# Performance work log

Hardware: AMD Instinct MI355X
Metric: run time of the kernel (lower is better)

The kernel has to match this reference:

```python
import jax, jax.numpy as jnp
import numpy as np

B, FEAT, H, W = 16, 64, 32, 32


def setup_inputs() -> dict:
    key = jax.random.key(0)
    ks = jax.random.split(key, 8)
    s = 0.05
    return {
        "x": jax.random.normal(ks[0], (B, 2 * FEAT, H, W), jnp.float32),
        # i2s_conv: MaskConv(2F -> 4F, 1x1, maskB with group=1 == all-ones), bias=False
        "w_i2s": jax.random.normal(ks[1], (4 * FEAT, 2 * FEAT), jnp.float32) * s,
        # left/right state-to-state Conv2d(F -> 4F, kernel (2,1)), with bias
        "w_left": jax.random.normal(ks[2], (4 * FEAT, FEAT, 2), jnp.float32) * s,
        "b_left": jax.random.normal(ks[3], (4 * FEAT,), jnp.float32) * s,
        "w_right": jax.random.normal(ks[4], (4 * FEAT, FEAT, 2), jnp.float32) * s,
        "b_right": jax.random.normal(ks[5], (4 * FEAT,), jnp.float32) * s,
        # skip_conv: MaskConv(F -> 2F, 1x1, maskB group=1 == plain conv), bias=True
        "w_skip": jax.random.normal(ks[6], (2 * FEAT, FEAT), jnp.float32) * s,
        "b_skip": jax.random.normal(ks[7], (2 * FEAT,), jnp.float32) * s,
    }


def _shift_right_w(a):  # F.pad(a,(1,0,...))[..., :-1]
    return jnp.pad(a, ((0, 0), (0, 0), (0, 0), (1, 0)))[:, :, :, :-1]


def _shift_left_w(a):  # F.pad(a,(0,1,...))[..., 1:]
    return jnp.pad(a, ((0, 0), (0, 0), (0, 0), (0, 1)))[:, :, :, 1:]


def _shift_down_h(a):  # pad one row on top, drop last row
    return jnp.pad(a, ((0, 0), (0, 0), (1, 0), (0, 0)))[:, :, :-1, :]


def _s2s(hprev, w, b, wshift):
    # pad(top=1, side=1) + Conv2d kernel (2,1) + crop one column, expressed as
    # two 1x1 contractions on width-shifted / (width+height)-shifted maps.
    hw = wshift(hprev)            # [B,F,H,W] shifted one column
    hd = _shift_down_h(hw)        # additionally shifted one row down
    return (jnp.einsum('bchw,oc->bohw', hd, w[:, :, 0])
            + jnp.einsum('bchw,oc->bohw', hw, w[:, :, 1])
            + b[None, :, None, None])


def _forward(x, w_i2s, w_left, b_left, w_right, b_right, w_skip, b_skip):
    b_, c2, h_, w_ = x.shape
    f = c2 // 2
    hmap = jnp.einsum('bchw,oc->bohw', x, w_i2s)  # [B,4F,H,W]
    left_h = hmap   # stew: input-to-state shared between directions
    right_h = hmap
    zeros = jnp.zeros((b_, f, h_, w_), x.dtype)

    def step(carry, _):
        lc, lh, rc, rh = carry
        pre = jax.nn.sigmoid(_s2s(lh, w_left, b_left, _shift_right_w) + left_h)
        o, fg, ig, g = jnp.split(pre, 4, axis=1)
        lc = fg * lc + ig * g
        lh = o * jnp.tanh(lc)
        pre = jax.nn.sigmoid(_s2s(rh, w_right, b_right, _shift_left_w) + right_h)
        o, fg, ig, g = jnp.split(pre, 4, axis=1)
        rc = fg * rc + ig * g
        rh = o * jnp.tanh(rc)
        return (lc, lh, rc, rh), None

    (lc, lh, rc, rh), _ = jax.lax.scan(step, (zeros, zeros, zeros, zeros), None, length=h_)
    rh = _shift_down_h(rh)  # unstew + shift right stream down one row
    out_h = lh + rh         # [B,F,H,W]
    skip = jnp.einsum('bchw,oc->bohw', out_h, w_skip) + b_skip[None, :, None, None]
    return x + skip


def reference(x, w_i2s, w_left, b_left, w_right, b_right, w_skip, b_skip):
    return _forward(x, w_i2s, w_left, b_left, w_right, b_right, w_skip, b_skip)
```

## Files before the change

kernel.cpp:

```cpp
#include <hip/hip_runtime.h>


using bf16   = __bf16;
using bf16x8 = __attribute__((ext_vector_type(8))) __bf16;
using f32x4  = __attribute__((ext_vector_type(4))) float;

#define SCOPE_AGENT __HIP_MEMORY_SCOPE_AGENT
#define LOG2E 1.4426950408889634f
#define K2E   2.8853900817779268f

__device__ __forceinline__ bf16x8 bzero8() {
  bf16x8 v;
#pragma unroll
  for (int e = 0; e < 8; ++e) v[e] = (bf16)0.0f;
  return v;
}
__device__ __forceinline__ unsigned short f2bu(float f) {
  bf16 b = (bf16)f;
  return __builtin_bit_cast(unsigned short, b);
}
__device__ __forceinline__ float bu2f(unsigned short u) {
  return __uint_as_float(((unsigned)u) << 16);
}

__global__ void prep_kernel(const float* __restrict__ w_i2s,
                            const float* __restrict__ w_left,
                            const float* __restrict__ w_right,
                            const float* __restrict__ w_skip,
                            bf16* __restrict__ WnI, bf16* __restrict__ WnL,
                            bf16* __restrict__ WnR, bf16* __restrict__ WnS) {
  int t = blockIdx.x * 256 + threadIdx.x;
  if (t < 32768) {
    WnI[t] = (bf16)w_i2s[t];
    int o = t >> 7, k = t & 127;
    int src = (k < 64) ? (o * 128 + k * 2) : (o * 128 + (k - 64) * 2 + 1);
    WnL[t] = (bf16)(w_left[src] * LOG2E);
    WnR[t] = (bf16)(w_right[src] * LOG2E);
    if (t < 8192) WnS[t] = (bf16)w_skip[t];
  }
}

__global__ __launch_bounds__(256, 2)
void hmap_kernel(const float* __restrict__ x, const bf16* __restrict__ Wn,
                 const float* __restrict__ bL, const float* __restrict__ bR,
                 ushort4* __restrict__ hmapL, ushort4* __restrict__ hmapR) {
  __shared__ __align__(16) bf16 At[64 * 128];
  const int tile = blockIdx.x;
  const int b = tile >> 4, h0 = (tile & 15) << 1;
  const int t = threadIdx.x;
  const float* xb = x + (size_t)(b * 128) * 1024 + h0 * 32;
#pragma unroll
  for (int i = 0; i < 8; ++i) {
    int idx = t + 256 * i;
    int cc = idx >> 4, m4 = idx & 15;
    f32x4 v = *(const f32x4*)(xb + (size_t)cc * 1024 + m4 * 4);
#pragma unroll
    for (int e = 0; e < 4; ++e) {
      int m = m4 * 4 + e;
      int kb = (cc * 2) ^ ((m & 7) << 4);
      *(bf16*)((char*)At + m * 256 + kb) = (bf16)v[e];
    }
  }
  __syncthreads();
  const int wv = t >> 6, l = t & 63;
  const int l15 = l & 15, lq = l >> 4;
  const int c = wv * 16 + l15;
  bf16x8 bfrag[4][4];
#pragma unroll
  for (int g = 0; g < 4; ++g)
#pragma unroll
    for (int kk = 0; kk < 4; ++kk)
      bfrag[g][kk] = *(const bf16x8*)(Wn + (g * 64 + c) * 128 + kk * 32 + lq * 8);
  float blq[4], brq[4];
#pragma unroll
  for (int g = 0; g < 4; ++g) {
    blq[g] = bL[g * 64 + c] * LOG2E;
    brq[g] = bR[g * 64 + c] * LOG2E;
  }
  f32x4 acc[4][4];
  const f32x4 fz = {0.f, 0.f, 0.f, 0.f};
#pragma unroll
  for (int ms = 0; ms < 4; ++ms)
#pragma unroll
    for (int g = 0; g < 4; ++g) acc[ms][g] = fz;
#pragma unroll
  for (int kk = 0; kk < 4; ++kk) {
#pragma unroll
    for (int ms = 0; ms < 4; ++ms) {
      int m = ms * 16 + l15;
      int kb = ((kk * 32 + lq * 8) * 2) ^ ((m & 7) << 4);
      bf16x8 a = *(const bf16x8*)((const char*)At + m * 256 + kb);
#pragma unroll
      for (int g = 0; g < 4; ++g)
        acc[ms][g] =
            __builtin_amdgcn_mfma_f32_16x16x32_bf16(a, bfrag[g][kk], acc[ms][g], 0, 0, 0);
    }
  }
  const int pix0 = tile * 64;
#pragma unroll
  for (int ms = 0; ms < 4; ++ms)
#pragma unroll
    for (int j = 0; j < 4; ++j) {
      int p = pix0 + ms * 16 + lq * 4 + j;
      ushort4 hl, hr;
      float a0 = acc[ms][0][j] * LOG2E, a1 = acc[ms][1][j] * LOG2E;
      float a2 = acc[ms][2][j] * LOG2E, a3 = acc[ms][3][j] * LOG2E;
      hl.x = f2bu(a0 + blq[0]); hl.y = f2bu(a1 + blq[1]);
      hl.z = f2bu(a2 + blq[2]); hl.w = f2bu(a3 + blq[3]);
      hr.x = f2bu(a0 + brq[0]); hr.y = f2bu(a1 + brq[1]);
      hr.z = f2bu(a2 + brq[2]); hr.w = f2bu(a3 + brq[3]);
      hmapL[(size_t)p * 64 + c] = hl;
      hmapR[(size_t)p * 64 + c] = hr;
    }
}

__global__ __launch_bounds__(512, 4)
void scan_kernel(bf16* __restrict__ lhLout, bf16* __restrict__ lhRout,
                 const ushort4* __restrict__ hmapL,
                 const ushort4* __restrict__ hmapR,
                 const bf16* __restrict__ WnL, const bf16* __restrict__ WnR,
                 bf16* __restrict__ ring, unsigned* __restrict__ prodFlag,
                 unsigned* __restrict__ consFlag) {
  __shared__ __align__(16) bf16 buf[2][3 * 32 * 64];
  __shared__ __align__(16) ushort4 hlds[64 * 64];
  const int blk = blockIdx.x;
  const int q = blk & 31, tl = blk >> 5;
  const bool right = (q & 1) != 0;
  const int b = q >> 1;
  const int r0 = tl * 2;
  const int t = threadIdx.x;
  const int dw = right ? 1 : -1;
  bf16* __restrict__ lout = right ? lhRout : lhLout;
  const bf16* __restrict__ Wn = right ? WnR : WnL;
  const ushort4* __restrict__ hsrc =
      (right ? hmapR : hmapL) + (size_t)(b * 1024 + r0 * 32) * 64;
  const int w8 = t >> 6, l = t & 63, l15 = l & 15, lq = l >> 4;
  const int wv = w8 & 3, mhalf = w8 >> 2;
  const int c = wv * 16 + l15;
  const int wb_ = mhalf * 16;

#pragma unroll
  for (int i = 0; i < 8; ++i) hlds[t + 512 * i] = hsrc[t + 512 * i];

#pragma unroll
  for (int i = 0; i < 2; ++i) {
    int idx = t + 512 * i;
    if (idx < 768) ((bf16x8*)buf[0])[idx] = bzero8();
  }
  if (t < 256) ((bf16x8*)buf[1])[t] = bzero8();

  bf16x8 bfrag[4][4];
#pragma unroll
  for (int g = 0; g < 4; ++g)
#pragma unroll
    for (int kk = 0; kk < 4; ++kk)
      bfrag[g][kk] = *(const bf16x8*)(Wn + (g * 64 + c) * 128 + kk * 32 + lq * 8);
  float lcA[4], lcB[4];
#pragma unroll
  for (int j = 0; j < 4; ++j) {
    lcA[j] = 0.0f;
    lcB[j] = 0.0f;
  }

  const unsigned* pBelow = prodFlag + (size_t)(blk - 32) * 32;
  const unsigned* cAbove = consFlag + (size_t)(blk + 32) * 32;
  unsigned* myProd = prodFlag + (size_t)blk * 32;
  unsigned* myCons = consFlag + (size_t)blk * 32;

  const int wsrc = wb_ + l15 + dw;
  const bool oob = (unsigned)wsrc >= 32u;
  const int wc = wsrc & 31;
  const int swz = (wc & 7) << 4;

  __syncthreads();

#pragma unroll 1
  for (int s = 0; s < 32; ++s) {
    bf16* curb = buf[s & 1];
    bf16* nxtb = buf[(s + 1) & 1];
    const bool consume = (tl > 0) && (s > 0);
    const bool publish = (tl < 15) && (s < 31);
    bf16* slotOut = ring + (size_t)(((s & 3) * 512) + blk) * 2048;

    if (publish && s >= 4) {
      const unsigned tgt = (unsigned)(s - 3);
      while (__hip_atomic_load(cAbove, __ATOMIC_RELAXED, SCOPE_AGENT) < tgt)
        __builtin_amdgcn_s_sleep(1);
    }

    {
      f32x4 acc[4];
      const f32x4 fz = {0.f, 0.f, 0.f, 0.f};
#pragma unroll
      for (int g = 0; g < 4; ++g) acc[g] = fz;
#pragma unroll
      for (int kk = 0; kk < 4; ++kk) {
        const int srcr = 1 + (kk >> 1);
        const int c0 = (kk & 1) * 32 + lq * 8;
        int aoff = ((srcr * 32 + wc) * 128 + c0 * 2) ^ swz;
        bf16x8 a = *(const bf16x8*)((const char*)curb + aoff);
        if (oob) a = bzero8();
#pragma unroll
        for (int g = 0; g < 4; ++g)
          acc[g] = __builtin_amdgcn_mfma_f32_16x16x32_bf16(a, bfrag[g][kk], acc[g], 0, 0, 0);
      }
#pragma unroll
      for (int j = 0; j < 4; ++j) {
        const int w = wb_ + lq * 4 + j;
        ushort4 hm = hlds[(32 + w) * 64 + c];
        float e0 = __builtin_amdgcn_exp2f(-(acc[0][j] + bu2f(hm.x)));
        float e1 = __builtin_amdgcn_exp2f(-(acc[1][j] + bu2f(hm.y)));
        float e2 = __builtin_amdgcn_exp2f(-(acc[2][j] + bu2f(hm.z)));
        float e3 = __builtin_amdgcn_exp2f(-(acc[3][j] + bu2f(hm.w)));
        float fg = __builtin_amdgcn_rcpf(1.0f + e1);
        float igg = __builtin_amdgcn_rcpf((1.0f + e2) * (1.0f + e3));
        float lcv = fg * lcA[j] + K2E * igg;
        lcA[j] = lcv;
        float ey = __builtin_amdgcn_exp2f(-lcv);
        float lh = (1.0f - ey) * __builtin_amdgcn_rcpf((1.0f + e0) * (1.0f + ey));
        bf16 vb = (bf16)lh;
        int woff = ((2 * 32 + w) * 128 + c * 2) ^ ((w & 7) << 4);
        *(bf16*)((char*)nxtb + woff) = vb;
        if (publish) {
          unsigned u = (unsigned)__builtin_bit_cast(unsigned short, vb);
          unsigned pv = (unsigned)__shfl_xor((int)u, 1);
          if ((l & 1) == 0) {
            unsigned dword = u | (pv << 16);
            __hip_atomic_store((unsigned*)(slotOut + w * 64 + (c & ~1)), dword,
                               __ATOMIC_RELAXED, SCOPE_AGENT);
          }
        }
      }
    }
    __syncthreads();
    if (publish && t == 0)
      __hip_atomic_store(myProd, (unsigned)(s + 1), __ATOMIC_RELAXED, SCOPE_AGENT);

    if (consume) {
      const unsigned tgt = (unsigned)s;
      while (__hip_atomic_load(pBelow, __ATOMIC_RELAXED, SCOPE_AGENT) < tgt)
        __builtin_amdgcn_s_sleep(1);
      if (t < 256) {
        const bf16* slotIn =
            ring + (size_t)((((s - 1) & 3) * 512) + (blk - 32)) * 2048;
        int w = t >> 3, c8 = t & 7;
        const unsigned long long* src =
            (const unsigned long long*)(slotIn + w * 64 + c8 * 8);
        unsigned long long d0 = __hip_atomic_load(src, __ATOMIC_RELAXED, SCOPE_AGENT);
        unsigned long long d1 = __hip_atomic_load(src + 1, __ATOMIC_RELAXED, SCOPE_AGENT);
        int off = (w * 128 + c8 * 16) ^ ((w & 7) << 4);
        *(unsigned long long*)((char*)curb + off) = d0;
        *(unsigned long long*)((char*)curb + off + 8) = d1;
      }
    }
    __syncthreads();
    if (consume && t == 0)
      __hip_atomic_store(myCons, (unsigned)s, __ATOMIC_RELAXED, SCOPE_AGENT);

    {
      f32x4 acc[4];
      const f32x4 fz = {0.f, 0.f, 0.f, 0.f};
#pragma unroll
      for (int g = 0; g < 4; ++g) acc[g] = fz;
#pragma unroll
      for (int kk = 0; kk < 4; ++kk) {
        const int srcr = kk >> 1;
        const int c0 = (kk & 1) * 32 + lq * 8;
        int aoff = ((srcr * 32 + wc) * 128 + c0 * 2) ^ swz;
        bf16x8 a = *(const bf16x8*)((const char*)curb + aoff);
        if (oob) a = bzero8();
#pragma unroll
        for (int g = 0; g < 4; ++g)
          acc[g] = __builtin_amdgcn_mfma_f32_16x16x32_bf16(a, bfrag[g][kk], acc[g], 0, 0, 0);
      }
#pragma unroll
      for (int j = 0; j < 4; ++j) {
        const int w = wb_ + lq * 4 + j;
        ushort4 hm = hlds[w * 64 + c];
        float e0 = __builtin_amdgcn_exp2f(-(acc[0][j] + bu2f(hm.x)));
        float e1 = __builtin_amdgcn_exp2f(-(acc[1][j] + bu2f(hm.y)));
        float e2 = __builtin_amdgcn_exp2f(-(acc[2][j] + bu2f(hm.z)));
        float e3 = __builtin_amdgcn_exp2f(-(acc[3][j] + bu2f(hm.w)));
        float fg = __builtin_amdgcn_rcpf(1.0f + e1);
        float igg = __builtin_amdgcn_rcpf((1.0f + e2) * (1.0f + e3));
        float lcv = fg * lcB[j] + K2E * igg;
        lcB[j] = lcv;
        float ey = __builtin_amdgcn_exp2f(-lcv);
        float lh = (1.0f - ey) * __builtin_amdgcn_rcpf((1.0f + e0) * (1.0f + ey));
        int woff = ((1 * 32 + w) * 128 + c * 2) ^ ((w & 7) << 4);
        *(bf16*)((char*)nxtb + woff) = (bf16)lh;
      }
    }
    __syncthreads();
  }

  {
    int R = 1 + (t >> 8), rem = t & 255;
    int w = rem >> 3, c8 = rem & 7;
    int off = ((R * 32 + w) * 128 + c8 * 16) ^ ((w & 7) << 4);
    bf16x8 v = *(const bf16x8*)((const char*)buf[0] + off);
    *(bf16x8*)(lout + (size_t)((b * 32 + r0 + R - 1) * 32 + w) * 64 + c8 * 8) = v;
  }
}

__global__ __launch_bounds__(256, 2)
void final_kernel(const float* __restrict__ x, const bf16* __restrict__ lhL,
                  const bf16* __restrict__ lhR, const bf16* __restrict__ Wn,
                  const float* __restrict__ b_skip, float* __restrict__ out) {
  __shared__ __align__(16) bf16 At[64 * 64];
  __shared__ __align__(16) float smemT[128 * 72];
  const int tile = blockIdx.x;
  const int b = tile >> 4, h0 = (tile & 15) << 1;
  const int t = threadIdx.x;
#pragma unroll
  for (int i = 0; i < 2; ++i) {
    int idx = t + 256 * i;
    int m = idx >> 3, c8 = idx & 7;
    int h = h0 + (m >> 5), w = m & 31;
    size_t p = (size_t)(b * 32 + h) * 32 + w;
    bf16x8 vL = *(const bf16x8*)(lhL + p * 64 + c8 * 8);
    bf16x8 v;
    if (h > 0) {
      bf16x8 vR = *(const bf16x8*)(lhR + (p - 32) * 64 + c8 * 8);
#pragma unroll
      for (int e = 0; e < 8; ++e) v[e] = (bf16)((float)vL[e] + (float)vR[e]);
    } else {
      v = vL;
    }
    int kb = (c8 * 16) ^ ((m & 7) << 4);
    *(bf16x8*)((char*)At + m * 128 + kb) = v;
  }
  __syncthreads();
  const int wv = t >> 6, l = t & 63;
  const int l15 = l & 15, lq = l >> 4;
  const int c = wv * 16 + l15;
  bf16x8 bfrag[2][2];
#pragma unroll
  for (int g = 0; g < 2; ++g)
#pragma unroll
    for (int kk = 0; kk < 2; ++kk)
      bfrag[g][kk] = *(const bf16x8*)(Wn + (g * 64 + c) * 64 + kk * 32 + lq * 8);
  f32x4 acc[4][2];
  const f32x4 fz = {0.f, 0.f, 0.f, 0.f};
#pragma unroll
  for (int ms = 0; ms < 4; ++ms)
#pragma unroll
    for (int g = 0; g < 2; ++g) acc[ms][g] = fz;
#pragma unroll
  for (int kk = 0; kk < 2; ++kk) {
#pragma unroll
    for (int ms = 0; ms < 4; ++ms) {
      int m = ms * 16 + l15;
      int kb = ((kk * 32 + lq * 8) * 2) ^ ((m & 7) << 4);
      bf16x8 a = *(const bf16x8*)((const char*)At + m * 128 + kb);
#pragma unroll
      for (int g = 0; g < 2; ++g)
        acc[ms][g] =
            __builtin_amdgcn_mfma_f32_16x16x32_bf16(a, bfrag[g][kk], acc[ms][g], 0, 0, 0);
    }
  }
  float bsk[2];
#pragma unroll
  for (int g = 0; g < 2; ++g) bsk[g] = b_skip[g * 64 + c];
#pragma unroll
  for (int ms = 0; ms < 4; ++ms)
#pragma unroll
    for (int g = 0; g < 2; ++g)
#pragma unroll
      for (int j = 0; j < 4; ++j) {
        int m = ms * 16 + lq * 4 + j;
        int n = g * 64 + c;
        smemT[n * 72 + m] = acc[ms][g][j] + bsk[g];
      }
  __syncthreads();
  const float* xb = x + (size_t)(b * 128) * 1024 + h0 * 32;
  float* ob = out + (size_t)(b * 128) * 1024 + h0 * 32;
#pragma unroll
  for (int i = 0; i < 8; ++i) {
    int idx = t + 256 * i;
    int o2 = idx >> 4, m4 = idx & 15;
    f32x4 s = *(const f32x4*)(&smemT[o2 * 72 + m4 * 4]);
    f32x4 xv = *(const f32x4*)(xb + (size_t)o2 * 1024 + m4 * 4);
#pragma unroll
    for (int e = 0; e < 4; ++e) s[e] += xv[e];
    *(f32x4*)(ob + (size_t)o2 * 1024 + m4 * 4) = s;
  }
}

extern "C" void kernel_launch(void* const* d_in, const int* in_sizes, int n_in,
                              void* d_out, int out_size, void* d_ws, size_t ws_size,
                              hipStream_t stream) {
  const float* x       = (const float*)d_in[0];
  const float* w_i2s   = (const float*)d_in[1];
  const float* w_left  = (const float*)d_in[2];
  const float* b_left  = (const float*)d_in[3];
  const float* w_right = (const float*)d_in[4];
  const float* b_right = (const float*)d_in[5];
  const float* w_skip  = (const float*)d_in[6];
  const float* b_skip  = (const float*)d_in[7];
  float* out = (float*)d_out;
  char* ws = (char*)d_ws;

  bf16*     lhL   = (bf16*)(ws + 0x0000000);
  bf16*     lhR   = (bf16*)(ws + 0x0200000);
  ushort4*  hmapL = (ushort4*)(ws + 0x0400000);
  ushort4*  hmapR = (ushort4*)(ws + 0x0C00000);
  bf16*     ring  = (bf16*)(ws + 0x1400000);
  unsigned* prodF = (unsigned*)(ws + 0x1C00000);
  unsigned* consF = (unsigned*)(ws + 0x1C10000);
  bf16*     WnI   = (bf16*)(ws + 0x1C20000);
  bf16*     WnL   = (bf16*)(ws + 0x1C30000);
  bf16*     WnR   = (bf16*)(ws + 0x1C40000);
  bf16*     WnS   = (bf16*)(ws + 0x1C50000);

  hipMemsetAsync(ws + 0x1C00000, 0, 0x20000, stream);
  prep_kernel<<<128, 256, 0, stream>>>(w_i2s, w_left, w_right, w_skip, WnI, WnL, WnR, WnS);
  hmap_kernel<<<256, 256, 0, stream>>>(x, WnI, b_left, b_right, hmapL, hmapR);
  scan_kernel<<<512, 512, 0, stream>>>(lhL, lhR, hmapL, hmapR, WnL, WnR,
                                       ring, prodF, consF);
  final_kernel<<<256, 256, 0, stream>>>(x, lhL, lhR, WnS, b_skip, out);
}
```

Measured before the change: 173.9 us.

## Hoist ring consume before first half-step, seed MFMA accumulators with hmap, pad LDS

The cross-block ring read for the row below now happens at the start of each step, spread over all 512 threads. This removes one __syncthreads per step and moves the consumer wait off the critical path between the two half-steps. The input-to-state hmap values are loaded straight into the MFMA accumulators, so the adds in the gate epilogue go away. The hmap LDS array gets a padded stride of 65 to reduce bank conflicts. In exchange, the wait on the producer now sits before the first half's compute, and the buffer-reuse ordering depends on the remaining barriers.

```diff
diff --git a/kernel.cpp b/kernel.cpp
--- a/kernel.cpp
+++ b/kernel.cpp
@@ -22,6 +22,8 @@
 __device__ __forceinline__ float bu2f(unsigned short u) {
   return __uint_as_float(((unsigned)u) << 16);
 }
+__device__ __forceinline__ float dw_lo(unsigned u) { return __uint_as_float(u << 16); }
+__device__ __forceinline__ float dw_hi(unsigned u) { return __uint_as_float(u & 0xffff0000u); }
 
 __global__ void prep_kernel(const float* __restrict__ w_i2s,
                             const float* __restrict__ w_left,
@@ -122,7 +124,7 @@
                  bf16* __restrict__ ring, unsigned* __restrict__ prodFlag,
                  unsigned* __restrict__ consFlag) {
   __shared__ __align__(16) bf16 buf[2][3 * 32 * 64];
-  __shared__ __align__(16) ushort4 hlds[64 * 64];
+  __shared__ __align__(16) ushort4 hlds[64 * 65];
   const int blk = blockIdx.x;
   const int q = blk & 31, tl = blk >> 5;
   const bool right = (q & 1) != 0;
@@ -140,8 +142,11 @@
   const int wb_ = mhalf * 16;
 
 #pragma unroll
-  for (int i = 0; i < 8; ++i) hlds[t + 512 * i] = hsrc[t + 512 * i];
-
+  for (int i = 0; i < 8; ++i) {
+    int idx = t + 512 * i;
+    int px = idx >> 6, cc = idx & 63;
+    hlds[px * 65 + cc] = hsrc[idx];
+  }
 #pragma unroll
   for (int i = 0; i < 2; ++i) {
     int idx = t + 512 * i;
@@ -182,6 +187,21 @@
     const bool publish = (tl < 15) && (s < 31);
     bf16* slotOut = ring + (size_t)(((s & 3) * 512) + blk) * 2048;
 
+    if (consume) {
+      const unsigned tgt = (unsigned)s;
+      while (__hip_atomic_load(pBelow, __ATOMIC_RELAXED, SCOPE_AGENT) < tgt)
+        __builtin_amdgcn_s_sleep(1);
+      const bf16* slotIn =
+          ring + (size_t)((((s - 1) & 3) * 512) + (blk - 32)) * 2048;
+      int w = t >> 4, c4 = t & 15;
+      const unsigned long long* src =
+          (const unsigned long long*)(slotIn + w * 64 + c4 * 8);
+      unsigned long long d0 = __hip_atomic_load(src, __ATOMIC_RELAXED, SCOPE_AGENT);
+      int off = (w * 128 + c4 * 16) ^ ((w & 7) << 4);
+      *(unsigned long long*)((char*)curb + off) = d0;
+      int w2 = 0;
+      (void)w2;
+    }
     if (publish && s >= 4) {
       const unsigned tgt = (unsigned)(s - 3);
       while (__hip_atomic_load(cAbove, __ATOMIC_RELAXED, SCOPE_AGENT) < tgt)
@@ -190,9 +210,16 @@
 
     {
       f32x4 acc[4];
-      const f32x4 fz = {0.f, 0.f, 0.f, 0.f};
-#pragma unroll
-      for (int g = 0; g < 4; ++g) acc[g] = fz;
+#pragma unroll
+      for (int j2 = 0; j2 < 2; ++j2) {
+        int w0 = wb_ + lq * 4 + j2 * 2;
+        ushort4 h0 = hlds[(32 + w0) * 65 + c];
+        ushort4 h1 = hlds[(32 + w0 + 1) * 65 + c];
+        acc[0][j2 * 2] = bu2f(h0.x); acc[0][j2 * 2 + 1] = bu2f(h1.x);
+        acc[1][j2 * 2] = bu2f(h0.y); acc[1][j2 * 2 + 1] = bu2f(h1.y);
+        acc[2][j2 * 2] = bu2f(h0.z); acc[2][j2 * 2 + 1] = bu2f(h1.z);
+        acc[3][j2 * 2] = bu2f(h0.w); acc[3][j2 * 2 + 1] = bu2f(h1.w);
+      }
 #pragma unroll
       for (int kk = 0; kk < 4; ++kk) {
         const int srcr = 1 + (kk >> 1);
@@ -207,11 +234,10 @@
 #pragma unroll
       for (int j = 0; j < 4; ++j) {
         const int w = wb_ + lq * 4 + j;
-        ushort4 hm = hlds[(32 + w) * 64 + c];
-        float e0 = __builtin_amdgcn_exp2f(-(acc[0][j] + bu2f(hm.x)));
-        float e1 = __builtin_amdgcn_exp2f(-(acc[1][j] + bu2f(hm.y)));
-        float e2 = __builtin_amdgcn_exp2f(-(acc[2][j] + bu2f(hm.z)));
-        float e3 = __builtin_amdgcn_exp2f(-(acc[3][j] + bu2f(hm.w)));
+        float e0 = __builtin_amdgcn_exp2f(-acc[0][j]);
+        float e1 = __builtin_amdgcn_exp2f(-acc[1][j]);
+        float e2 = __builtin_amdgcn_exp2f(-acc[2][j]);
+        float e3 = __builtin_amdgcn_exp2f(-acc[3][j]);
         float fg = __builtin_amdgcn_rcpf(1.0f + e1);
         float igg = __builtin_amdgcn_rcpf((1.0f + e2) * (1.0f + e3));
         float lcv = fg * lcA[j] + K2E * igg;
@@ -235,33 +261,21 @@
     __syncthreads();
     if (publish && t == 0)
       __hip_atomic_store(myProd, (unsigned)(s + 1), __ATOMIC_RELAXED, SCOPE_AGENT);
-
-    if (consume) {
-      const unsigned tgt = (unsigned)s;
-      while (__hip_atomic_load(pBelow, __ATOMIC_RELAXED, SCOPE_AGENT) < tgt)
-        __builtin_amdgcn_s_sleep(1);
-      if (t < 256) {
-        const bf16* slotIn =
-            ring + (size_t)((((s - 1) & 3) * 512) + (blk - 32)) * 2048;
-        int w = t >> 3, c8 = t & 7;
-        const unsigned long long* src =
-            (const unsigned long long*)(slotIn + w * 64 + c8 * 8);
-        unsigned long long d0 = __hip_atomic_load(src, __ATOMIC_RELAXED, SCOPE_AGENT);
-        unsigned long long d1 = __hip_atomic_load(src + 1, __ATOMIC_RELAXED, SCOPE_AGENT);
-        int off = (w * 128 + c8 * 16) ^ ((w & 7) << 4);
-        *(unsigned long long*)((char*)curb + off) = d0;
-        *(unsigned long long*)((char*)curb + off + 8) = d1;
-      }
-    }
-    __syncthreads();
-    if (consume && t == 0)
+    if (consume && t == 64)
       __hip_atomic_store(myCons, (unsigned)s, __ATOMIC_RELAXED, SCOPE_AGENT);
 
     {
       f32x4 acc[4];
-      const f32x4 fz = {0.f, 0.f, 0.f, 0.f};
-#pragma unroll
-      for (int g = 0; g < 4; ++g) acc[g] = fz;
+#pragma unroll
+      for (int j2 = 0; j2 < 2; ++j2) {
+        int w0 = wb_ + lq * 4 + j2 * 2;
+        ushort4 h0 = hlds[w0 * 65 + c];
+        ushort4 h1 = hlds[(w0 + 1) * 65 + c];
+        acc[0][j2 * 2] = bu2f(h0.x); acc[0][j2 * 2 + 1] = bu2f(h1.x);
+        acc[1][j2 * 2] = bu2f(h0.y); acc[1][j2 * 2 + 1] = bu2f(h1.y);
+        acc[2][j2 * 2] = bu2f(h0.z); acc[2][j2 * 2 + 1] = bu2f(h1.z);
+        acc[3][j2 * 2] = bu2f(h0.w); acc[3][j2 * 2 + 1] = bu2f(h1.w);
+      }
 #pragma unroll
       for (int kk = 0; kk < 4; ++kk) {
         const int srcr = kk >> 1;
@@ -276,11 +290,10 @@
 #pragma unroll
       for (int j = 0; j < 4; ++j) {
         const int w = wb_ + lq * 4 + j;
-        ushort4 hm = hlds[w * 64 + c];
-        float e0 = __builtin_amdgcn_exp2f(-(acc[0][j] + bu2f(hm.x)));
-        float e1 = __builtin_amdgcn_exp2f(-(acc[1][j] + bu2f(hm.y)));
-        float e2 = __builtin_amdgcn_exp2f(-(acc[2][j] + bu2f(hm.z)));
-        float e3 = __builtin_amdgcn_exp2f(-(acc[3][j] + bu2f(hm.w)));
+        float e0 = __builtin_amdgcn_exp2f(-acc[0][j]);
+        float e1 = __builtin_amdgcn_exp2f(-acc[1][j]);
+        float e2 = __builtin_amdgcn_exp2f(-acc[2][j]);
+        float e3 = __builtin_amdgcn_exp2f(-acc[3][j]);
         float fg = __builtin_amdgcn_rcpf(1.0f + e1);
         float igg = __builtin_amdgcn_rcpf((1.0f + e2) * (1.0f + e3));
         float lcv = fg * lcB[j] + K2E * igg;
```

Result: no change. 174.0 us (+0.1%).
